# Kernel optimization log

Measured on AMD Instinct MI355X. Metric: run time of the kernel, lower is better.

Reference implementation:

```python
import jax, jax.numpy as jnp
import numpy as np

QLEN, MLEN, BSZ = 1024, 1024, 4
D_MODEL, N_HEAD, D_HEAD, D_INNER = 1024, 16, 64, 4096
KLEN = QLEN + MLEN  # = rlen
LN_EPS = 1e-5


def setup_inputs() -> dict:
    key = jax.random.key(0)
    ks = jax.random.split(key, 16)
    s = 0.02
    nhd = N_HEAD * D_HEAD
    inp = {
        "dec_inp": jax.random.normal(ks[0], (QLEN, BSZ, D_MODEL), jnp.float32),
        "r": jax.random.normal(ks[1], (KLEN, D_MODEL), jnp.float32),
        "r_w_bias": jax.random.normal(ks[2], (N_HEAD, D_HEAD), jnp.float32) * s,
        "r_r_bias": jax.random.normal(ks[3], (N_HEAD, D_HEAD), jnp.float32) * s,
        "mems": jax.random.normal(ks[4], (MLEN, BSZ, D_MODEL), jnp.float32),
        # causal mask with memory: position j visible to query i iff j <= i + MLEN
        "dec_attn_mask": (jnp.arange(KLEN)[None, :] > (jnp.arange(QLEN)[:, None] + MLEN))[:, :, None],
        # parameters
        "qkv_w": jax.random.normal(ks[5], (D_MODEL, 3 * nhd), jnp.float32) * s,
        "r_w": jax.random.normal(ks[6], (D_MODEL, nhd), jnp.float32) * s,
        "o_w": jax.random.normal(ks[7], (nhd, D_MODEL), jnp.float32) * s,
        "ln1_w": jnp.ones((D_MODEL,), jnp.float32),
        "ln1_b": jnp.zeros((D_MODEL,), jnp.float32),
        "ln2_w": jnp.ones((D_MODEL,), jnp.float32),
        "ln2_b": jnp.zeros((D_MODEL,), jnp.float32),
        "ff_w1": jax.random.normal(ks[8], (D_MODEL, D_INNER), jnp.float32) * s,
        "ff_b1": jnp.zeros((D_INNER,), jnp.float32),
        "ff_w2": jax.random.normal(ks[9], (D_INNER, D_MODEL), jnp.float32) * s,
        "ff_b2": jnp.zeros((D_MODEL,), jnp.float32),
    }
    return inp


def _layer_norm(x, w, b):
    mu = jnp.mean(x, axis=-1, keepdims=True)
    var = jnp.mean(jnp.square(x - mu), axis=-1, keepdims=True)
    return (x - mu) * jax.lax.rsqrt(var + LN_EPS) * w + b


def _rel_shift(x):
    # x: [qlen, rlen, bsz, n_head] -- Transformer-XL pad/reshape shift
    q, rl = x.shape[0], x.shape[1]
    zero_pad = jnp.zeros((q, 1) + x.shape[2:], x.dtype)
    x_padded = jnp.concatenate([zero_pad, x], axis=1)
    x_padded = x_padded.reshape((rl + 1, q) + x.shape[2:])
    return x_padded[1:].reshape(x.shape)


def reference(dec_inp, r, r_w_bias, r_r_bias, mems, dec_attn_mask,
              qkv_w, r_w, o_w, ln1_w, ln1_b, ln2_w, ln2_b,
              ff_w1, ff_b1, ff_w2, ff_b2):
    qlen, bsz = dec_inp.shape[0], dec_inp.shape[1]
    nhd = N_HEAD * D_HEAD
    scale = 1.0 / (D_HEAD ** 0.5)

    cat = jnp.concatenate([mems, dec_inp], axis=0)          # [klen, b, d]
    w_heads = cat @ qkv_w                                   # [klen, b, 3*nhd]
    w_head_q, w_head_k, w_head_v = jnp.split(w_heads, 3, axis=-1)
    w_head_q = w_head_q[-qlen:]                             # [qlen, b, nhd]
    klen = w_head_k.shape[0]

    w_head_q = w_head_q.reshape(qlen, bsz, N_HEAD, D_HEAD)
    w_head_k = w_head_k.reshape(klen, bsz, N_HEAD, D_HEAD)
    w_head_v = w_head_v.reshape(klen, bsz, N_HEAD, D_HEAD)
    r_head_k = (r @ r_w).reshape(-1, N_HEAD, D_HEAD)        # [rlen, n, d]

    AC = jnp.einsum('ibnd,jbnd->ijbn', w_head_q + r_w_bias, w_head_k)
    BD = jnp.einsum('ibnd,jnd->ijbn', w_head_q + r_r_bias, r_head_k)
    BD = _rel_shift(BD)

    attn_score = (AC + BD) * scale                          # [q, k, b, n]
    attn_score = jnp.where(dec_attn_mask[:, :, :, None], -jnp.inf, attn_score)
    attn_prob = jax.nn.softmax(attn_score, axis=1)

    attn_vec = jnp.einsum('ijbn,jbnd->ibnd', attn_prob, w_head_v)
    attn_out = attn_vec.reshape(qlen, bsz, nhd) @ o_w       # [q, b, d]

    output = _layer_norm(dec_inp + attn_out, ln1_w, ln1_b)
    ff = jax.nn.relu(output @ ff_w1 + ff_b1) @ ff_w2 + ff_b2
    return _layer_norm(output + ff, ln2_w, ln2_b)
```

## Files before the change

### kernel.cpp

```cpp
#include <hip/hip_runtime.h>
#include <hip/hip_bf16.h>
#include <math.h>

#define QLEN 1024
#define MLEN 1024
#define BSZ 4
#define KLEN 2048
#define NH 16
#define DH 64
#define DM 1024
#define DI 4096
#define NHD 1024
#define LN_EPS 1e-5f

typedef short bf16x8 __attribute__((ext_vector_type(8)));
typedef float f32x4 __attribute__((ext_vector_type(4)));
typedef unsigned int uint4v __attribute__((ext_vector_type(4)));

__device__ __forceinline__ float bf2f(unsigned short u) {
    union { unsigned u32; float f; } x; x.u32 = ((unsigned)u) << 16; return x.f;
}
__device__ __forceinline__ unsigned short f2bf(float f) {
    __hip_bfloat16 h = __float2bfloat16(f);
    return *(unsigned short*)&h;
}

static const size_t OFF_CATB  = 0;
static const size_t OFF_VTG   = 0;
static const size_t OFF_WHB   = 16777216;
static const size_t OFF_RB    = 67108864;
static const size_t OFF_RHKB  = 71303168;
static const size_t OFF_AVB   = 75497472;
static const size_t OFF_TMP   = 83886080;
static const size_t OFF_LN1F  = 100663296;
static const size_t OFF_LN1B  = 117440512;
static const size_t OFF_FFHB  = 125829120;
static const size_t OFF_QKVWT = 159383552;
static const size_t OFF_RWT   = 165675008;
static const size_t OFF_OWT   = 167772160;
static const size_t OFF_FFW1T = 169869312;
static const size_t OFF_FFW2T = 178257920;

__global__ __launch_bounds__(256) void cast_cat(const float* __restrict__ mems,
                                                const float* __restrict__ dec,
                                                unsigned short* __restrict__ out) {
    size_t i8 = ((size_t)blockIdx.x * 256 + threadIdx.x) * 8;
    const size_t half = (size_t)MLEN * BSZ * DM;
    const float* src = (i8 < half) ? (mems + i8) : (dec + (i8 - half));
    float4 v0 = *(const float4*)src;
    float4 v1 = *(const float4*)(src + 4);
    ushort4 o0 = {f2bf(v0.x), f2bf(v0.y), f2bf(v0.z), f2bf(v0.w)};
    ushort4 o1 = {f2bf(v1.x), f2bf(v1.y), f2bf(v1.z), f2bf(v1.w)};
    *(ushort4*)&out[i8] = o0;
    *(ushort4*)&out[i8 + 4] = o1;
}

__global__ __launch_bounds__(256) void cast_f32_bf16(const float* __restrict__ in,
                                                     unsigned short* __restrict__ out) {
    size_t i8 = ((size_t)blockIdx.x * 256 + threadIdx.x) * 8;
    float4 v0 = *(const float4*)(in + i8);
    float4 v1 = *(const float4*)(in + i8 + 4);
    ushort4 o0 = {f2bf(v0.x), f2bf(v0.y), f2bf(v0.z), f2bf(v0.w)};
    ushort4 o1 = {f2bf(v1.x), f2bf(v1.y), f2bf(v1.z), f2bf(v1.w)};
    *(ushort4*)&out[i8] = o0;
    *(ushort4*)&out[i8 + 4] = o1;
}

__global__ __launch_bounds__(256) void transpose_cast_all(
        const float* __restrict__ qkv_w, const float* __restrict__ r_w,
        const float* __restrict__ o_w,  const float* __restrict__ ff_w1,
        const float* __restrict__ ff_w2,
        unsigned short* __restrict__ qkvwT, unsigned short* __restrict__ rwT,
        unsigned short* __restrict__ owT, unsigned short* __restrict__ ffw1T,
        unsigned short* __restrict__ ffw2T) {
    __shared__ float tile[32][33];
    const int bid = blockIdx.x;
    const float* in; unsigned short* out; int K, N, nx, lid;
    if (bid < 3072)      { in = qkv_w; out = qkvwT; K = 1024; N = 3072; nx = 96;  lid = bid; }
    else if (bid < 4096) { in = r_w;   out = rwT;   K = 1024; N = 1024; nx = 32;  lid = bid - 3072; }
    else if (bid < 5120) { in = o_w;   out = owT;   K = 1024; N = 1024; nx = 32;  lid = bid - 4096; }
    else if (bid < 9216) { in = ff_w1; out = ffw1T; K = 1024; N = 4096; nx = 128; lid = bid - 5120; }
    else                 { in = ff_w2; out = ffw2T; K = 4096; N = 1024; nx = 32;  lid = bid - 9216; }
    const int n0 = (lid % nx) * 32;
    const int k0 = (lid / nx) * 32;
    const int t = threadIdx.x;
    const int r = t >> 3;
    const int c0 = (t & 7) << 2;
    float4 v = *(const float4*)&in[(size_t)(k0 + r) * N + n0 + c0];
    tile[r][c0 + 0] = v.x; tile[r][c0 + 1] = v.y;
    tile[r][c0 + 2] = v.z; tile[r][c0 + 3] = v.w;
    __syncthreads();
    ushort4 o = {f2bf(tile[c0 + 0][r]), f2bf(tile[c0 + 1][r]),
                 f2bf(tile[c0 + 2][r]), f2bf(tile[c0 + 3][r])};
    *(ushort4*)&out[(size_t)(n0 + r) * K + k0 + c0] = o;
}

__global__ __launch_bounds__(256) void gemm_bf16(const unsigned short* __restrict__ A,
                                                 const unsigned short* __restrict__ Bt,
                                                 const float* __restrict__ bias,
                                                 void* __restrict__ C,
                                                 int M, int N, int K, int flags) {
    __shared__ __align__(16) unsigned short As[128 * 64];
    __shared__ __align__(16) unsigned short Bs[128 * 64];

    const int tid = threadIdx.x;
    const int w = tid >> 6, l = tid & 63;
    const int wr = w >> 1, wc = w & 1;
    const int row0 = blockIdx.y * 128;
    const int col0 = blockIdx.x * 128;

    f32x4 acc[4][4] = {};

    uint4v ra[4], rb[4];
    {
#pragma unroll
        for (int q = 0; q < 4; ++q) {
            int f = q * 256 + tid, r = f >> 3, c = f & 7;
            ra[q] = *(const uint4v*)&A[(size_t)(row0 + r) * K + c * 8];
            rb[q] = *(const uint4v*)&Bt[(size_t)(col0 + r) * K + c * 8];
        }
    }

    const int nt = K >> 6;
    for (int kt = 0; kt < nt; ++kt) {
        __syncthreads();
#pragma unroll
        for (int q = 0; q < 4; ++q) {
            int f = q * 256 + tid, r = f >> 3, c = f & 7;
            int sw = (c ^ (r & 7)) << 3;
            *(uint4v*)&As[r * 64 + sw] = ra[q];
            *(uint4v*)&Bs[r * 64 + sw] = rb[q];
        }
        __syncthreads();
        if (kt + 1 < nt) {
            const int k0 = (kt + 1) << 6;
#pragma unroll
            for (int q = 0; q < 4; ++q) {
                int f = q * 256 + tid, r = f >> 3, c = f & 7;
                ra[q] = *(const uint4v*)&A[(size_t)(row0 + r) * K + k0 + c * 8];
                rb[q] = *(const uint4v*)&Bt[(size_t)(col0 + r) * K + k0 + c * 8];
            }
        }
#pragma unroll
        for (int ks = 0; ks < 2; ++ks) {
            bf16x8 a[4], bfr[4];
#pragma unroll
            for (int m = 0; m < 4; ++m) {
                int arow = wr * 64 + m * 16 + (l & 15);
                int chunk = (ks * 4 + (l >> 4)) ^ (arow & 7);
                a[m] = *(const bf16x8*)&As[arow * 64 + chunk * 8];
            }
#pragma unroll
            for (int n = 0; n < 4; ++n) {
                int brow = wc * 64 + n * 16 + (l & 15);
                int chunk = (ks * 4 + (l >> 4)) ^ (brow & 7);
                bfr[n] = *(const bf16x8*)&Bs[brow * 64 + chunk * 8];
            }
#pragma unroll
            for (int m = 0; m < 4; ++m)
#pragma unroll
                for (int n = 0; n < 4; ++n)
                    acc[m][n] = __builtin_amdgcn_mfma_f32_16x16x32_bf16(a[m], bfr[n], acc[m][n], 0, 0, 0);
        }
    }

#pragma unroll
    for (int n = 0; n < 4; ++n) {
        const int ccol = col0 + wc * 64 + n * 16 + (l & 15);
        const float bv = (flags & 1) ? bias[ccol] : 0.0f;
#pragma unroll
        for (int m = 0; m < 4; ++m) {
            const int crow0 = row0 + wr * 64 + m * 16 + ((l >> 4) << 2);
#pragma unroll
            for (int reg = 0; reg < 4; ++reg) {
                float v = acc[m][n][reg] + bv;
                if (flags & 2) v = fmaxf(v, 0.0f);
                if (flags & 4)
                    ((unsigned short*)C)[(size_t)(crow0 + reg) * N + ccol] = f2bf(v);
                else
                    ((float*)C)[(size_t)(crow0 + reg) * N + ccol] = v;
            }
        }
    }
}

__global__ __launch_bounds__(256) void vtrans(const unsigned short* __restrict__ whb,
                                              unsigned short* __restrict__ vtg) {
    __shared__ unsigned short tile[64][72];
    const int bn = blockIdx.y;
    const int b = bn >> 4, n = bn & 15, nb = n * 64;
    const int jt0 = blockIdx.x * 64;
    const int tid = threadIdx.x;
#pragma unroll
    for (int g = 0; g < 2; ++g) {
        int f = g * 256 + tid;
        int key = f >> 3, c = f & 7;
        uint4v v = *(const uint4v*)&whb[((size_t)(jt0 + key) * 4 + b) * 3072 + 2048 + nb + c * 8];
        *(uint4v*)&tile[key][c * 8] = v;
    }
    __syncthreads();
#pragma unroll
    for (int g = 0; g < 2; ++g) {
        int f = g * 256 + tid;
        int d = f >> 3, ck = f & 7;
        unsigned short tmp[8];
#pragma unroll
        for (int e = 0; e < 8; ++e) tmp[e] = tile[ck * 8 + e][d];
        *(uint4v*)&vtg[(size_t)bn * 131072 + (size_t)d * 2048 + jt0 + ck * 8] = *(uint4v*)tmp;
    }
}

__global__ __launch_bounds__(512) void flash_attn_mfma(const unsigned short* __restrict__ whb,
                                                       const unsigned short* __restrict__ rhkb,
                                                       const unsigned short* __restrict__ vtg,
                                                       const float* __restrict__ r_w_bias,
                                                       const float* __restrict__ r_r_bias,
                                                       unsigned short* __restrict__ avb) {
    const int bid = blockIdx.x;
    const int bn = bid >> 3;
    const int z = bid & 7;
    const int bx = (z & 1) ? (z >> 1) : 7 - (z >> 1);
    const int b = bn >> 4, n = bn & 15, nb = n * 64;
    const int i0 = bx << 7;
    const int tid = threadIdx.x;
    const int wq = tid >> 6;
    const int lane = tid & 63;
    const int rg = lane >> 4;
    const int lc = lane & 15;
    const int m7 = lc & 7;

    __shared__ __align__(16) unsigned short Ks[4096];
    __shared__ __align__(16) unsigned short Rs[16384];
    __shared__ __align__(16) unsigned short Vt[4096];
    __shared__ __align__(16) unsigned short SCR[8][1408];

    bf16x8 qac0, qac1, qbd0, qbd1;
    {
        const int qrow = MLEN + i0 + wq * 16 + lc;
        const unsigned short* qp = whb + ((size_t)qrow * 4 + b) * 3072 + nb + rg * 8;
        bf16x8 q0 = *(const bf16x8*)(qp);
        bf16x8 q1 = *(const bf16x8*)(qp + 32);
        const float* wbp = r_w_bias + nb + rg * 8;
        const float* rbp = r_r_bias + nb + rg * 8;
#pragma unroll
        for (int e = 0; e < 8; ++e) {
            const float v0 = bf2f((unsigned short)q0[e]);
            const float v1 = bf2f((unsigned short)q1[e]);
            qac0[e] = (short)f2bf((v0 + wbp[e]) * 0.125f);
            qbd0[e] = (short)f2bf((v0 + rbp[e]) * 0.125f);
            qac1[e] = (short)f2bf((v1 + wbp[32 + e]) * 0.125f);
            qbd1[e] = (short)f2bf((v1 + rbp[32 + e]) * 0.125f);
        }
    }

    f32x4 Oacc[4] = {};
    float mrun = -INFINITY, lrun = 0.f;

    const int ntiles = 2 * bx + 18;
    const int wbase_off = 112 - 16 * wq;

    const int srow = tid >> 3;
    const int sc = tid & 7;
    unsigned short* scr = &SCR[wq][0];

    uint4v pk, pv, pr3[3];
    {
        pk = *(const uint4v*)&whb[((size_t)srow * 4 + b) * 3072 + 1024 + nb + sc * 8];
        pv = *(const uint4v*)&vtg[(size_t)bn * 131072 + (size_t)srow * 2048 + sc * 8];
        const int relbase0 = 896 - i0;
#pragma unroll
        for (int p = 0; p < 3; ++p) {
            const int a = relbase0 + p * 64 + srow;
            pr3[p] = *(const uint4v*)&rhkb[(size_t)a * 1024 + nb + sc * 8];
        }
    }

    for (int kt = 0; kt < ntiles; ++kt) {
        const int jt0 = kt << 6;
        const int relbase = jt0 - i0 + 896;
        __syncthreads();

        *(uint4v*)&Ks[srow * 64 + ((sc ^ (srow & 7)) << 3)] = pk;
        *(uint4v*)&Vt[srow * 64 + ((sc ^ (srow & 7)) << 3)] = pv;
        if (kt == 0) {
#pragma unroll
            for (int p = 0; p < 3; ++p) {
                const int a = relbase + p * 64 + srow;
                const int dst = ((a >> 6) & 3) * 4096 + (a & 63) * 64 + ((sc ^ (a & 7)) << 3);
                *(uint4v*)&Rs[dst] = pr3[p];
            }
        } else {
            const int a = relbase + 128 + srow;
            const int dst = ((a >> 6) & 3) * 4096 + (a & 63) * 64 + ((sc ^ (a & 7)) << 3);
            *(uint4v*)&Rs[dst] = pr3[0];
        }
        if (kt + 1 < ntiles) {
            const int jn = jt0 + 64;
            pk = *(const uint4v*)&whb[((size_t)(jn + srow) * 4 + b) * 3072 + 1024 + nb + sc * 8];
            pv = *(const uint4v*)&vtg[(size_t)bn * 131072 + (size_t)srow * 2048 + jn + sc * 8];
            int a = relbase + 192 + srow;
            if (a > 2047) a = 2047;
            pr3[0] = *(const uint4v*)&rhkb[(size_t)a * 1024 + nb + sc * 8];
        }
        __syncthreads();

        f32x4 S[4];
        __builtin_amdgcn_s_setprio(1);
#pragma unroll
        for (int nf = 0; nf < 4; ++nf) {
            const int row = nf * 16 + lc;
            const bf16x8 kf0 = *(const bf16x8*)&Ks[row * 64 + ((rg ^ m7) << 3)];
            const bf16x8 kf1 = *(const bf16x8*)&Ks[row * 64 + (((4 + rg) ^ m7) << 3)];
            f32x4 zz = {0.f, 0.f, 0.f, 0.f};
            zz = __builtin_amdgcn_mfma_f32_16x16x32_bf16(kf0, qac0, zz, 0, 0, 0);
            S[nf] = __builtin_amdgcn_mfma_f32_16x16x32_bf16(kf1, qac1, zz, 0, 0, 0);
        }
        __builtin_amdgcn_s_setprio(0);

        const int wbase = relbase + wbase_off;
#pragma unroll
        for (int g = 0; g < 5; ++g) {
            const int a = wbase + g * 16 + lc;
            const int rbase = ((a >> 6) & 3) * 4096 + (a & 63) * 64;
            const bf16x8 rf0 = *(const bf16x8*)&Rs[rbase + ((rg ^ m7) << 3)];
            const bf16x8 rf1 = *(const bf16x8*)&Rs[rbase + (((4 + rg) ^ m7) << 3)];
            f32x4 bd = {0.f, 0.f, 0.f, 0.f};
            bd = __builtin_amdgcn_mfma_f32_16x16x32_bf16(rf0, qbd0, bd, 0, 0, 0);
            bd = __builtin_amdgcn_mfma_f32_16x16x32_bf16(rf1, qbd1, bd, 0, 0, 0);
            ushort4 p4 = {f2bf(bd[0]), f2bf(bd[1]), f2bf(bd[2]), f2bf(bd[3])};
            *(ushort4*)&scr[lc * 88 + g * 16 + rg * 4] = p4;
        }

        const bool needmask = (wbase + 78 > 2047);
        float tmax = -INFINITY;
#pragma unroll
        for (int nf = 0; nf < 4; ++nf) {
#pragma unroll
            for (int r = 0; r < 4; ++r) {
                const int wb_ = 15 + nf * 16 + rg * 4 + r - lc;
                float s = S[nf][r] + bf2f(scr[lc * 88 + wb_]);
                if (needmask) s = (wbase + wb_ <= 2047) ? s : -INFINITY;
                S[nf][r] = s;
                tmax = fmaxf(tmax, s);
            }
        }

        tmax = fmaxf(tmax, __shfl_xor(tmax, 16));
        tmax = fmaxf(tmax, __shfl_xor(tmax, 32));
        const float mn = fmaxf(mrun, tmax);
        const float ef = __expf(mrun - mn);
        mrun = mn;
        float rsum = 0.f;
#pragma unroll
        for (int nf = 0; nf < 4; ++nf) {
#pragma unroll
            for (int r = 0; r < 4; ++r) {
                const float p = __expf(S[nf][r] - mn);
                S[nf][r] = p;
                rsum += p;
            }
        }
        rsum += __shfl_xor(rsum, 16);
        rsum += __shfl_xor(rsum, 32);
        lrun = lrun * ef + rsum;
        if (__any(ef < 1.0f)) {
#pragma unroll
            for (int nf = 0; nf < 4; ++nf)
#pragma unroll
                for (int r = 0; r < 4; ++r) Oacc[nf][r] *= ef;
        }

#pragma unroll
        for (int nf = 0; nf < 4; ++nf) {
            ushort4 pw = {f2bf(S[nf][0]), f2bf(S[nf][1]), f2bf(S[nf][2]), f2bf(S[nf][3])};
            const int chunk = nf * 2 + (rg >> 1);
            *(ushort4*)&scr[lc * 88 + ((chunk ^ m7) << 3) + ((rg & 1) << 2)] = pw;
        }

        {
            const bf16x8 pf0 = *(const bf16x8*)&scr[lc * 88 + ((rg ^ m7) << 3)];
            const bf16x8 pf1 = *(const bf16x8*)&scr[lc * 88 + (((4 + rg) ^ m7) << 3)];
            __builtin_amdgcn_s_setprio(1);
#pragma unroll
            for (int nf = 0; nf < 4; ++nf) {
                const int row = nf * 16 + lc;
                const bf16x8 vf0 = *(const bf16x8*)&Vt[row * 64 + ((rg ^ m7) << 3)];
                const bf16x8 vf1 = *(const bf16x8*)&Vt[row * 64 + (((4 + rg) ^ m7) << 3)];
                Oacc[nf] = __builtin_amdgcn_mfma_f32_16x16x32_bf16(vf0, pf0, Oacc[nf], 0, 0, 0);
                Oacc[nf] = __builtin_amdgcn_mfma_f32_16x16x32_bf16(vf1, pf1, Oacc[nf], 0, 0, 0);
            }
            __builtin_amdgcn_s_setprio(0);
        }
    }

    const float inv = 1.0f / lrun;
    const int qg = i0 + wq * 16 + lc;
#pragma unroll
    for (int nf = 0; nf < 4; ++nf) {
        ushort4 o = {f2bf(Oacc[nf][0] * inv), f2bf(Oacc[nf][1] * inv),
                     f2bf(Oacc[nf][2] * inv), f2bf(Oacc[nf][3] * inv)};
        *(ushort4*)&avb[((size_t)qg * 4 + b) * 1024 + nb + nf * 16 + rg * 4] = o;
    }
}

__global__ __launch_bounds__(256) void add_ln_kernel(const float* __restrict__ a,
                                                     const float* __restrict__ b,
                                                     const float* __restrict__ w,
                                                     const float* __restrict__ bias,
                                                     float* __restrict__ out,
                                                     unsigned short* __restrict__ out_bf) {
    const int row = blockIdx.x;
    const int t = threadIdx.x;
    const int c0 = t << 2;
    __shared__ float red[256];

    const float4 av = *(const float4*)&a[(size_t)row * DM + c0];
    const float4 bv = *(const float4*)&b[(size_t)row * DM + c0];
    float x0 = av.x + bv.x, x1 = av.y + bv.y, x2 = av.z + bv.z, x3 = av.w + bv.w;

    red[t] = x0 + x1 + x2 + x3;
    __syncthreads();
    for (int off = 128; off > 0; off >>= 1) {
        if (t < off) red[t] += red[t + off];
        __syncthreads();
    }
    const float mu = red[0] * (1.0f / DM);
    __syncthreads();

    const float d0 = x0 - mu, d1 = x1 - mu, d2 = x2 - mu, d3 = x3 - mu;
    red[t] = d0 * d0 + d1 * d1 + d2 * d2 + d3 * d3;
    __syncthreads();
    for (int off = 128; off > 0; off >>= 1) {
        if (t < off) red[t] += red[t + off];
        __syncthreads();
    }
    const float rstd = rsqrtf(red[0] * (1.0f / DM) + LN_EPS);

    const float4 wv = *(const float4*)&w[c0];
    const float4 bsv = *(const float4*)&bias[c0];
    float4 o = {d0 * rstd * wv.x + bsv.x, d1 * rstd * wv.y + bsv.y,
                d2 * rstd * wv.z + bsv.z, d3 * rstd * wv.w + bsv.w};
    *(float4*)&out[(size_t)row * DM + c0] = o;
    if (out_bf) {
        ushort4 ob = {f2bf(o.x), f2bf(o.y), f2bf(o.z), f2bf(o.w)};
        *(ushort4*)&out_bf[(size_t)row * DM + c0] = ob;
    }
}

extern "C" void kernel_launch(void* const* d_in, const int* in_sizes, int n_in,
                              void* d_out, int out_size, void* d_ws, size_t ws_size,
                              hipStream_t stream) {
    const float* dec_inp  = (const float*)d_in[0];
    const float* r        = (const float*)d_in[1];
    const float* r_w_bias = (const float*)d_in[2];
    const float* r_r_bias = (const float*)d_in[3];
    const float* mems     = (const float*)d_in[4];
    const float* qkv_w    = (const float*)d_in[6];
    const float* r_w      = (const float*)d_in[7];
    const float* o_w      = (const float*)d_in[8];
    const float* ln1_w    = (const float*)d_in[9];
    const float* ln1_b    = (const float*)d_in[10];
    const float* ln2_w    = (const float*)d_in[11];
    const float* ln2_b    = (const float*)d_in[12];
    const float* ff_w1    = (const float*)d_in[13];
    const float* ff_b1    = (const float*)d_in[14];
    const float* ff_w2    = (const float*)d_in[15];
    const float* ff_b2    = (const float*)d_in[16];
    float* out = (float*)d_out;
    char* ws = (char*)d_ws;

    unsigned short* catb  = (unsigned short*)(ws + OFF_CATB);
    unsigned short* vtg   = (unsigned short*)(ws + OFF_VTG);
    unsigned short* whb   = (unsigned short*)(ws + OFF_WHB);
    unsigned short* rb    = (unsigned short*)(ws + OFF_RB);
    unsigned short* rhkb  = (unsigned short*)(ws + OFF_RHKB);
    unsigned short* avb   = (unsigned short*)(ws + OFF_AVB);
    float*          tmp   = (float*)(ws + OFF_TMP);
    float*          ln1f  = (float*)(ws + OFF_LN1F);
    unsigned short* ln1b  = (unsigned short*)(ws + OFF_LN1B);
    unsigned short* ffhb  = (unsigned short*)(ws + OFF_FFHB);
    unsigned short* qkvwT = (unsigned short*)(ws + OFF_QKVWT);
    unsigned short* rwT   = (unsigned short*)(ws + OFF_RWT);
    unsigned short* owT   = (unsigned short*)(ws + OFF_OWT);
    unsigned short* ffw1T = (unsigned short*)(ws + OFF_FFW1T);
    unsigned short* ffw2T = (unsigned short*)(ws + OFF_FFW2T);

    cast_cat<<<dim3(4096), 256, 0, stream>>>(mems, dec_inp, catb);
    cast_f32_bf16<<<dim3(1024), 256, 0, stream>>>(r, rb);
    transpose_cast_all<<<dim3(13312), 256, 0, stream>>>(
        qkv_w, r_w, o_w, ff_w1, ff_w2, qkvwT, rwT, owT, ffw1T, ffw2T);

    gemm_bf16<<<dim3(24, 64), 256, 0, stream>>>(catb, qkvwT, nullptr, whb,
                                                KLEN * BSZ, 3 * NHD, DM, 4);
    gemm_bf16<<<dim3(8, 16), 256, 0, stream>>>(rb, rwT, nullptr, rhkb,
                                               KLEN, NHD, DM, 4);

    vtrans<<<dim3(32, 64), 256, 0, stream>>>(whb, vtg);

    flash_attn_mfma<<<dim3(512), 512, 0, stream>>>(
        whb, rhkb, vtg, r_w_bias, r_r_bias, avb);

    gemm_bf16<<<dim3(8, 32), 256, 0, stream>>>(avb, owT, nullptr, tmp,
                                               QLEN * BSZ, DM, NHD, 0);
    add_ln_kernel<<<dim3(QLEN * BSZ), 256, 0, stream>>>(
        dec_inp, tmp, ln1_w, ln1_b, ln1f, ln1b);
    gemm_bf16<<<dim3(32, 32), 256, 0, stream>>>(ln1b, ffw1T, ff_b1, ffhb,
                                                QLEN * BSZ, DI, DM, 1 | 2 | 4);
    gemm_bf16<<<dim3(8, 32), 256, 0, stream>>>(ffhb, ffw2T, ff_b2, tmp,
                                               QLEN * BSZ, DM, DI, 1);
    add_ln_kernel<<<dim3(QLEN * BSZ), 256, 0, stream>>>(
        ln1f, tmp, ln2_w, ln2_b, out, nullptr);
}
```

Baseline: 402.8 us.

## Load K, V and R MFMA fragments directly from global memory, dropping LDS staging

The attention kernel no longer stages K, V^T and relative-position R tiles through shared memory with register prefetch and two block barriers per tile. Each wave now reads its MFMA operand fragments straight from global memory, clamping R indices at the end of the sequence. This removes the barriers and LDS traffic but makes the 8 waves each re-read the same K/V/R data from cache/HBM, with strided, less coalesced accesses and no software prefetch.

Measured after the change: 623.2 us. +54.7%, slower.

```diff
diff --git a/kernel.cpp b/kernel.cpp
--- a/kernel.cpp
+++ b/kernel.cpp
@@ -229,9 +229,6 @@
     const int lc = lane & 15;
     const int m7 = lc & 7;
 
-    __shared__ __align__(16) unsigned short Ks[4096];
-    __shared__ __align__(16) unsigned short Rs[16384];
-    __shared__ __align__(16) unsigned short Vt[4096];
     __shared__ __align__(16) unsigned short SCR[8][1408];
 
     bf16x8 qac0, qac1, qbd0, qbd1;
@@ -258,72 +255,37 @@
 
     const int ntiles = 2 * bx + 18;
     const int wbase_off = 112 - 16 * wq;
-
-    const int srow = tid >> 3;
-    const int sc = tid & 7;
     unsigned short* scr = &SCR[wq][0];
 
-    uint4v pk, pv, pr3[3];
-    {
-        pk = *(const uint4v*)&whb[((size_t)srow * 4 + b) * 3072 + 1024 + nb + sc * 8];
-        pv = *(const uint4v*)&vtg[(size_t)bn * 131072 + (size_t)srow * 2048 + sc * 8];
-        const int relbase0 = 896 - i0;
-#pragma unroll
-        for (int p = 0; p < 3; ++p) {
-            const int a = relbase0 + p * 64 + srow;
-            pr3[p] = *(const uint4v*)&rhkb[(size_t)a * 1024 + nb + sc * 8];
-        }
-    }
+    const unsigned short* kfrag = whb + (size_t)b * 3072 + 1024 + nb + rg * 8 + (size_t)lc * 12288;
+    const unsigned short* vfrag = vtg + (size_t)bn * 131072 + (size_t)lc * 2048 + rg * 8;
+    const unsigned short* rfrag = rhkb + nb + rg * 8;
 
     for (int kt = 0; kt < ntiles; ++kt) {
         const int jt0 = kt << 6;
         const int relbase = jt0 - i0 + 896;
-        __syncthreads();
-
-        *(uint4v*)&Ks[srow * 64 + ((sc ^ (srow & 7)) << 3)] = pk;
-        *(uint4v*)&Vt[srow * 64 + ((sc ^ (srow & 7)) << 3)] = pv;
-        if (kt == 0) {
-#pragma unroll
-            for (int p = 0; p < 3; ++p) {
-                const int a = relbase + p * 64 + srow;
-                const int dst = ((a >> 6) & 3) * 4096 + (a & 63) * 64 + ((sc ^ (a & 7)) << 3);
-                *(uint4v*)&Rs[dst] = pr3[p];
-            }
-        } else {
-            const int a = relbase + 128 + srow;
-            const int dst = ((a >> 6) & 3) * 4096 + (a & 63) * 64 + ((sc ^ (a & 7)) << 3);
-            *(uint4v*)&Rs[dst] = pr3[0];
-        }
-        if (kt + 1 < ntiles) {
-            const int jn = jt0 + 64;
-            pk = *(const uint4v*)&whb[((size_t)(jn + srow) * 4 + b) * 3072 + 1024 + nb + sc * 8];
-            pv = *(const uint4v*)&vtg[(size_t)bn * 131072 + (size_t)srow * 2048 + jn + sc * 8];
-            int a = relbase + 192 + srow;
-            if (a > 2047) a = 2047;
-            pr3[0] = *(const uint4v*)&rhkb[(size_t)a * 1024 + nb + sc * 8];
-        }
-        __syncthreads();
+        const int wbase = relbase + wbase_off;
 
         f32x4 S[4];
         __builtin_amdgcn_s_setprio(1);
 #pragma unroll
         for (int nf = 0; nf < 4; ++nf) {
-            const int row = nf * 16 + lc;
-            const bf16x8 kf0 = *(const bf16x8*)&Ks[row * 64 + ((rg ^ m7) << 3)];
-            const bf16x8 kf1 = *(const bf16x8*)&Ks[row * 64 + (((4 + rg) ^ m7) << 3)];
+            const unsigned short* kp = kfrag + (size_t)(jt0 + nf * 16) * 12288;
+            const bf16x8 kf0 = *(const bf16x8*)(kp);
+            const bf16x8 kf1 = *(const bf16x8*)(kp + 32);
             f32x4 zz = {0.f, 0.f, 0.f, 0.f};
             zz = __builtin_amdgcn_mfma_f32_16x16x32_bf16(kf0, qac0, zz, 0, 0, 0);
             S[nf] = __builtin_amdgcn_mfma_f32_16x16x32_bf16(kf1, qac1, zz, 0, 0, 0);
         }
         __builtin_amdgcn_s_setprio(0);
 
-        const int wbase = relbase + wbase_off;
 #pragma unroll
         for (int g = 0; g < 5; ++g) {
-            const int a = wbase + g * 16 + lc;
-            const int rbase = ((a >> 6) & 3) * 4096 + (a & 63) * 64;
-            const bf16x8 rf0 = *(const bf16x8*)&Rs[rbase + ((rg ^ m7) << 3)];
-            const bf16x8 rf1 = *(const bf16x8*)&Rs[rbase + (((4 + rg) ^ m7) << 3)];
+            int a = wbase + g * 16 + lc;
+            if (a > 2047) a = 2047;
+            const unsigned short* rp = rfrag + (size_t)a * 1024;
+            const bf16x8 rf0 = *(const bf16x8*)(rp);
+            const bf16x8 rf1 = *(const bf16x8*)(rp + 32);
             f32x4 bd = {0.f, 0.f, 0.f, 0.f};
             bd = __builtin_amdgcn_mfma_f32_16x16x32_bf16(rf0, qbd0, bd, 0, 0, 0);
             bd = __builtin_amdgcn_mfma_f32_16x16x32_bf16(rf1, qbd1, bd, 0, 0, 0);
@@ -383,9 +345,9 @@
             __builtin_amdgcn_s_setprio(1);
 #pragma unroll
             for (int nf = 0; nf < 4; ++nf) {
-                const int row = nf * 16 + lc;
-                const bf16x8 vf0 = *(const bf16x8*)&Vt[row * 64 + ((rg ^ m7) << 3)];
-                const bf16x8 vf1 = *(const bf16x8*)&Vt[row * 64 + (((4 + rg) ^ m7) << 3)];
+                const unsigned short* vp = vfrag + (size_t)(nf * 16) * 2048 + jt0;
+                const bf16x8 vf0 = *(const bf16x8*)(vp);
+                const bf16x8 vf1 = *(const bf16x8*)(vp + 32);
                 Oacc[nf] = __builtin_amdgcn_mfma_f32_16x16x32_bf16(vf0, pf0, Oacc[nf], 0, 0, 0);
                 Oacc[nf] = __builtin_amdgcn_mfma_f32_16x16x32_bf16(vf1, pf1, Oacc[nf], 0, 0, 0);
             }
```

## Split attention key range into two halves per block with merge kernel

Applied to the files above, without the earlier changes.

Each attention block now handles two jobs. Each job covers half the key tiles of a query block, and the jobs pair a short query block with a long one so work is balanced. Partial unnormalized outputs and running max/sum are written in fp32 and combined by a new merge kernel. The pairing is meant to fix load imbalance from the causal triangle, at the cost of extra fp32 partial traffic and one more kernel launch. The o-proj and FF2 GEMMs also now write bf16 intermediates instead of fp32, which lowers bandwidth but loses some precision.

Measured after the change: 396.2 us. No clear change (-1.6%).

```diff
diff --git a/kernel.cpp b/kernel.cpp
--- a/kernel.cpp
+++ b/kernel.cpp
@@ -31,7 +31,8 @@
 static const size_t OFF_RB    = 67108864;
 static const size_t OFF_RHKB  = 71303168;
 static const size_t OFF_AVB   = 75497472;
-static const size_t OFF_TMP   = 83886080;
+static const size_t OFF_TMPB  = 83886080;
+static const size_t OFF_ML    = 92274688;
 static const size_t OFF_LN1F  = 100663296;
 static const size_t OFF_LN1B  = 117440512;
 static const size_t OFF_FFHB  = 125829120;
@@ -215,13 +216,12 @@
                                                        const unsigned short* __restrict__ vtg,
                                                        const float* __restrict__ r_w_bias,
                                                        const float* __restrict__ r_r_bias,
-                                                       unsigned short* __restrict__ avb) {
+                                                       float* __restrict__ opart,
+                                                       float* __restrict__ ml) {
     const int bid = blockIdx.x;
     const int bn = bid >> 3;
-    const int z = bid & 7;
-    const int bx = (z & 1) ? (z >> 1) : 7 - (z >> 1);
+    const int kk0 = bid & 7;
     const int b = bn >> 4, n = bn & 15, nb = n * 64;
-    const int i0 = bx << 7;
     const int tid = threadIdx.x;
     const int wq = tid >> 6;
     const int lane = tid & 63;
@@ -234,177 +234,215 @@
     __shared__ __align__(16) unsigned short Vt[4096];
     __shared__ __align__(16) unsigned short SCR[8][1408];
 
-    bf16x8 qac0, qac1, qbd0, qbd1;
-    {
-        const int qrow = MLEN + i0 + wq * 16 + lc;
-        const unsigned short* qp = whb + ((size_t)qrow * 4 + b) * 3072 + nb + rg * 8;
-        bf16x8 q0 = *(const bf16x8*)(qp);
-        bf16x8 q1 = *(const bf16x8*)(qp + 32);
-        const float* wbp = r_w_bias + nb + rg * 8;
-        const float* rbp = r_r_bias + nb + rg * 8;
-#pragma unroll
-        for (int e = 0; e < 8; ++e) {
-            const float v0 = bf2f((unsigned short)q0[e]);
-            const float v1 = bf2f((unsigned short)q1[e]);
-            qac0[e] = (short)f2bf((v0 + wbp[e]) * 0.125f);
-            qbd0[e] = (short)f2bf((v0 + rbp[e]) * 0.125f);
-            qac1[e] = (short)f2bf((v1 + wbp[32 + e]) * 0.125f);
-            qbd1[e] = (short)f2bf((v1 + rbp[32 + e]) * 0.125f);
-        }
-    }
-
-    f32x4 Oacc[4] = {};
-    float mrun = -INFINITY, lrun = 0.f;
-
-    const int ntiles = 2 * bx + 18;
     const int wbase_off = 112 - 16 * wq;
-
     const int srow = tid >> 3;
     const int sc = tid & 7;
     unsigned short* scr = &SCR[wq][0];
 
-    uint4v pk, pv, pr3[3];
-    {
-        pk = *(const uint4v*)&whb[((size_t)srow * 4 + b) * 3072 + 1024 + nb + sc * 8];
-        pv = *(const uint4v*)&vtg[(size_t)bn * 131072 + (size_t)srow * 2048 + sc * 8];
-        const int relbase0 = 896 - i0;
-#pragma unroll
-        for (int p = 0; p < 3; ++p) {
-            const int a = relbase0 + p * 64 + srow;
-            pr3[p] = *(const uint4v*)&rhkb[(size_t)a * 1024 + nb + sc * 8];
-        }
-    }
-
-    for (int kt = 0; kt < ntiles; ++kt) {
-        const int jt0 = kt << 6;
-        const int relbase = jt0 - i0 + 896;
-        __syncthreads();
-
-        *(uint4v*)&Ks[srow * 64 + ((sc ^ (srow & 7)) << 3)] = pk;
-        *(uint4v*)&Vt[srow * 64 + ((sc ^ (srow & 7)) << 3)] = pv;
-        if (kt == 0) {
+    for (int job = 0; job < 2; ++job) {
+        const int h = job;
+        const int bx = job ? (7 - kk0) : kk0;
+        const int i0 = bx << 7;
+        const int halfn = bx + 9;
+        const int kt0 = h * halfn;
+        const int ktend = kt0 + halfn;
+
+        bf16x8 qac0, qac1, qbd0, qbd1;
+        {
+            const int qrow = MLEN + i0 + wq * 16 + lc;
+            const unsigned short* qp = whb + ((size_t)qrow * 4 + b) * 3072 + nb + rg * 8;
+            bf16x8 q0 = *(const bf16x8*)(qp);
+            bf16x8 q1 = *(const bf16x8*)(qp + 32);
+            const float* wbp = r_w_bias + nb + rg * 8;
+            const float* rbp = r_r_bias + nb + rg * 8;
+#pragma unroll
+            for (int e = 0; e < 8; ++e) {
+                const float v0 = bf2f((unsigned short)q0[e]);
+                const float v1 = bf2f((unsigned short)q1[e]);
+                qac0[e] = (short)f2bf((v0 + wbp[e]) * 0.125f);
+                qbd0[e] = (short)f2bf((v0 + rbp[e]) * 0.125f);
+                qac1[e] = (short)f2bf((v1 + wbp[32 + e]) * 0.125f);
+                qbd1[e] = (short)f2bf((v1 + rbp[32 + e]) * 0.125f);
+            }
+        }
+
+        f32x4 Oacc[4] = {};
+        float mrun = -INFINITY, lrun = 0.f;
+
+        uint4v pk, pv, pr3[3];
+        {
+            const int j0 = kt0 << 6;
+            pk = *(const uint4v*)&whb[((size_t)(j0 + srow) * 4 + b) * 3072 + 1024 + nb + sc * 8];
+            pv = *(const uint4v*)&vtg[(size_t)bn * 131072 + (size_t)srow * 2048 + j0 + sc * 8];
+            const int relst = j0 - i0 + 896;
 #pragma unroll
             for (int p = 0; p < 3; ++p) {
-                const int a = relbase + p * 64 + srow;
+                int a = relst + p * 64 + srow;
+                if (a > 2047) a = 2047;
+                pr3[p] = *(const uint4v*)&rhkb[(size_t)a * 1024 + nb + sc * 8];
+            }
+        }
+
+        for (int kt = kt0; kt < ktend; ++kt) {
+            const int jt0 = kt << 6;
+            const int relbase = jt0 - i0 + 896;
+            __syncthreads();
+
+            *(uint4v*)&Ks[srow * 64 + ((sc ^ (srow & 7)) << 3)] = pk;
+            *(uint4v*)&Vt[srow * 64 + ((sc ^ (srow & 7)) << 3)] = pv;
+            if (kt == kt0) {
+#pragma unroll
+                for (int p = 0; p < 3; ++p) {
+                    int a = relbase + p * 64 + srow;
+                    if (a > 2047) a = 2047;
+                    const int dst = ((a >> 6) & 3) * 4096 + (a & 63) * 64 + ((sc ^ (a & 7)) << 3);
+                    *(uint4v*)&Rs[dst] = pr3[p];
+                }
+            } else {
+                int a = relbase + 128 + srow;
+                if (a > 2047) a = 2047;
                 const int dst = ((a >> 6) & 3) * 4096 + (a & 63) * 64 + ((sc ^ (a & 7)) << 3);
-                *(uint4v*)&Rs[dst] = pr3[p];
-            }
-        } else {
-            const int a = relbase + 128 + srow;
-            const int dst = ((a >> 6) & 3) * 4096 + (a & 63) * 64 + ((sc ^ (a & 7)) << 3);
-            *(uint4v*)&Rs[dst] = pr3[0];
-        }
-        if (kt + 1 < ntiles) {
-            const int jn = jt0 + 64;
-            pk = *(const uint4v*)&whb[((size_t)(jn + srow) * 4 + b) * 3072 + 1024 + nb + sc * 8];
-            pv = *(const uint4v*)&vtg[(size_t)bn * 131072 + (size_t)srow * 2048 + jn + sc * 8];
-            int a = relbase + 192 + srow;
-            if (a > 2047) a = 2047;
-            pr3[0] = *(const uint4v*)&rhkb[(size_t)a * 1024 + nb + sc * 8];
-        }
-        __syncthreads();
-
-        f32x4 S[4];
-        __builtin_amdgcn_s_setprio(1);
-#pragma unroll
-        for (int nf = 0; nf < 4; ++nf) {
-            const int row = nf * 16 + lc;
-            const bf16x8 kf0 = *(const bf16x8*)&Ks[row * 64 + ((rg ^ m7) << 3)];
-            const bf16x8 kf1 = *(const bf16x8*)&Ks[row * 64 + (((4 + rg) ^ m7) << 3)];
-            f32x4 zz = {0.f, 0.f, 0.f, 0.f};
-            zz = __builtin_amdgcn_mfma_f32_16x16x32_bf16(kf0, qac0, zz, 0, 0, 0);
-            S[nf] = __builtin_amdgcn_mfma_f32_16x16x32_bf16(kf1, qac1, zz, 0, 0, 0);
-        }
-        __builtin_amdgcn_s_setprio(0);
-
-        const int wbase = relbase + wbase_off;
-#pragma unroll
-        for (int g = 0; g < 5; ++g) {
-            const int a = wbase + g * 16 + lc;
-            const int rbase = ((a >> 6) & 3) * 4096 + (a & 63) * 64;
-            const bf16x8 rf0 = *(const bf16x8*)&Rs[rbase + ((rg ^ m7) << 3)];
-            const bf16x8 rf1 = *(const bf16x8*)&Rs[rbase + (((4 + rg) ^ m7) << 3)];
-            f32x4 bd = {0.f, 0.f, 0.f, 0.f};
-            bd = __builtin_amdgcn_mfma_f32_16x16x32_bf16(rf0, qbd0, bd, 0, 0, 0);
-            bd = __builtin_amdgcn_mfma_f32_16x16x32_bf16(rf1, qbd1, bd, 0, 0, 0);
-            ushort4 p4 = {f2bf(bd[0]), f2bf(bd[1]), f2bf(bd[2]), f2bf(bd[3])};
-            *(ushort4*)&scr[lc * 88 + g * 16 + rg * 4] = p4;
-        }
-
-        const bool needmask = (wbase + 78 > 2047);
-        float tmax = -INFINITY;
-#pragma unroll
-        for (int nf = 0; nf < 4; ++nf) {
-#pragma unroll
-            for (int r = 0; r < 4; ++r) {
-                const int wb_ = 15 + nf * 16 + rg * 4 + r - lc;
-                float s = S[nf][r] + bf2f(scr[lc * 88 + wb_]);
-                if (needmask) s = (wbase + wb_ <= 2047) ? s : -INFINITY;
-                S[nf][r] = s;
-                tmax = fmaxf(tmax, s);
-            }
-        }
-
-        tmax = fmaxf(tmax, __shfl_xor(tmax, 16));
-        tmax = fmaxf(tmax, __shfl_xor(tmax, 32));
-        const float mn = fmaxf(mrun, tmax);
-        const float ef = __expf(mrun - mn);
-        mrun = mn;
-        float rsum = 0.f;
-#pragma unroll
-        for (int nf = 0; nf < 4; ++nf) {
-#pragma unroll
-            for (int r = 0; r < 4; ++r) {
-                const float p = __expf(S[nf][r] - mn);
-                S[nf][r] = p;
-                rsum += p;
-            }
-        }
-        rsum += __shfl_xor(rsum, 16);
-        rsum += __shfl_xor(rsum, 32);
-        lrun = lrun * ef + rsum;
-        if (__any(ef < 1.0f)) {
-#pragma unroll
-            for (int nf = 0; nf < 4; ++nf)
-#pragma unroll
-                for (int r = 0; r < 4; ++r) Oacc[nf][r] *= ef;
-        }
-
-#pragma unroll
-        for (int nf = 0; nf < 4; ++nf) {
-            ushort4 pw = {f2bf(S[nf][0]), f2bf(S[nf][1]), f2bf(S[nf][2]), f2bf(S[nf][3])};
-            const int chunk = nf * 2 + (rg >> 1);
-            *(ushort4*)&scr[lc * 88 + ((chunk ^ m7) << 3) + ((rg & 1) << 2)] = pw;
-        }
-
-        {
-            const bf16x8 pf0 = *(const bf16x8*)&scr[lc * 88 + ((rg ^ m7) << 3)];
-            const bf16x8 pf1 = *(const bf16x8*)&scr[lc * 88 + (((4 + rg) ^ m7) << 3)];
+                *(uint4v*)&Rs[dst] = pr3[0];
+            }
+            if (kt + 1 < ktend) {
+                const int jn = jt0 + 64;
+                pk = *(const uint4v*)&whb[((size_t)(jn + srow) * 4 + b) * 3072 + 1024 + nb + sc * 8];
+                pv = *(const uint4v*)&vtg[(size_t)bn * 131072 + (size_t)srow * 2048 + jn + sc * 8];
+                int a = relbase + 192 + srow;
+                if (a > 2047) a = 2047;
+                pr3[0] = *(const uint4v*)&rhkb[(size_t)a * 1024 + nb + sc * 8];
+            }
+            __syncthreads();
+
+            f32x4 S[4];
             __builtin_amdgcn_s_setprio(1);
 #pragma unroll
             for (int nf = 0; nf < 4; ++nf) {
                 const int row = nf * 16 + lc;
-                const bf16x8 vf0 = *(const bf16x8*)&Vt[row * 64 + ((rg ^ m7) << 3)];
-                const bf16x8 vf1 = *(const bf16x8*)&Vt[row * 64 + (((4 + rg) ^ m7) << 3)];
-                Oacc[nf] = __builtin_amdgcn_mfma_f32_16x16x32_bf16(vf0, pf0, Oacc[nf], 0, 0, 0);
-                Oacc[nf] = __builtin_amdgcn_mfma_f32_16x16x32_bf16(vf1, pf1, Oacc[nf], 0, 0, 0);
+                const bf16x8 kf0 = *(const bf16x8*)&Ks[row * 64 + ((rg ^ m7) << 3)];
+                const bf16x8 kf1 = *(const bf16x8*)&Ks[row * 64 + (((4 + rg) ^ m7) << 3)];
+                f32x4 zz = {0.f, 0.f, 0.f, 0.f};
+                zz = __builtin_amdgcn_mfma_f32_16x16x32_bf16(kf0, qac0, zz, 0, 0, 0);
+                S[nf] = __builtin_amdgcn_mfma_f32_16x16x32_bf16(kf1, qac1, zz, 0, 0, 0);
             }
             __builtin_amdgcn_s_setprio(0);
-        }
-    }
-
-    const float inv = 1.0f / lrun;
-    const int qg = i0 + wq * 16 + lc;
-#pragma unroll
-    for (int nf = 0; nf < 4; ++nf) {
-        ushort4 o = {f2bf(Oacc[nf][0] * inv), f2bf(Oacc[nf][1] * inv),
-                     f2bf(Oacc[nf][2] * inv), f2bf(Oacc[nf][3] * inv)};
-        *(ushort4*)&avb[((size_t)qg * 4 + b) * 1024 + nb + nf * 16 + rg * 4] = o;
-    }
+
+            const int wbase = relbase + wbase_off;
+#pragma unroll
+            for (int g = 0; g < 5; ++g) {
+                const int a = wbase + g * 16 + lc;
+                const int rbase = ((a >> 6) & 3) * 4096 + (a & 63) * 64;
+                const bf16x8 rf0 = *(const bf16x8*)&Rs[rbase + ((rg ^ m7) << 3)];
+                const bf16x8 rf1 = *(const bf16x8*)&Rs[rbase + (((4 + rg) ^ m7) << 3)];
+                f32x4 bd = {0.f, 0.f, 0.f, 0.f};
+                bd = __builtin_amdgcn_mfma_f32_16x16x32_bf16(rf0, qbd0, bd, 0, 0, 0);
+                bd = __builtin_amdgcn_mfma_f32_16x16x32_bf16(rf1, qbd1, bd, 0, 0, 0);
+                ushort4 p4 = {f2bf(bd[0]), f2bf(bd[1]), f2bf(bd[2]), f2bf(bd[3])};
+                *(ushort4*)&scr[lc * 88 + g * 16 + rg * 4] = p4;
+            }
+
+            const bool needmask = (wbase + 78 > 2047);
+            float tmax = -INFINITY;
+#pragma unroll
+            for (int nf = 0; nf < 4; ++nf) {
+#pragma unroll
+                for (int r = 0; r < 4; ++r) {
+                    const int wb_ = 15 + nf * 16 + rg * 4 + r - lc;
+                    float s = S[nf][r] + bf2f(scr[lc * 88 + wb_]);
+                    if (needmask) s = (wbase + wb_ <= 2047) ? s : -INFINITY;
+                    S[nf][r] = s;
+                    tmax = fmaxf(tmax, s);
+                }
+            }
+
+            tmax = fmaxf(tmax, __shfl_xor(tmax, 16));
+            tmax = fmaxf(tmax, __shfl_xor(tmax, 32));
+            const float mn = fmaxf(mrun, tmax);
+            const float ef = __expf(mrun - mn);
+            mrun = mn;
+            float rsum = 0.f;
+#pragma unroll
+            for (int nf = 0; nf < 4; ++nf) {
+#pragma unroll
+                for (int r = 0; r < 4; ++r) {
+                    const float p = __expf(S[nf][r] - mn);
+                    S[nf][r] = p;
+                    rsum += p;
+                }
+            }
+            rsum += __shfl_xor(rsum, 16);
+            rsum += __shfl_xor(rsum, 32);
+            lrun = lrun * ef + rsum;
+            if (__any(ef < 1.0f)) {
+#pragma unroll
+                for (int nf = 0; nf < 4; ++nf)
+#pragma unroll
+                    for (int r = 0; r < 4; ++r) Oacc[nf][r] *= ef;
+            }
+
+#pragma unroll
+            for (int nf = 0; nf < 4; ++nf) {
+                ushort4 pw = {f2bf(S[nf][0]), f2bf(S[nf][1]), f2bf(S[nf][2]), f2bf(S[nf][3])};
+                const int chunk = nf * 2 + (rg >> 1);
+                *(ushort4*)&scr[lc * 88 + ((chunk ^ m7) << 3) + ((rg & 1) << 2)] = pw;
+            }
+
+            {
+                const bf16x8 pf0 = *(const bf16x8*)&scr[lc * 88 + ((rg ^ m7) << 3)];
+                const bf16x8 pf1 = *(const bf16x8*)&scr[lc * 88 + (((4 + rg) ^ m7) << 3)];
+                __builtin_amdgcn_s_setprio(1);
+#pragma unroll
+                for (int nf = 0; nf < 4; ++nf) {
+                    const int row = nf * 16 + lc;
+                    const bf16x8 vf0 = *(const bf16x8*)&Vt[row * 64 + ((rg ^ m7) << 3)];
+                    const bf16x8 vf1 = *(const bf16x8*)&Vt[row * 64 + (((4 + rg) ^ m7) << 3)];
+                    Oacc[nf] = __builtin_amdgcn_mfma_f32_16x16x32_bf16(vf0, pf0, Oacc[nf], 0, 0, 0);
+                    Oacc[nf] = __builtin_amdgcn_mfma_f32_16x16x32_bf16(vf1, pf1, Oacc[nf], 0, 0, 0);
+                }
+                __builtin_amdgcn_s_setprio(0);
+            }
+        }
+
+        const int qg = i0 + wq * 16 + lc;
+        const int rowf = qg * 4 + b;
+        float* op = opart + (size_t)h * 4194304 + (size_t)rowf * 1024 + nb;
+#pragma unroll
+        for (int nf = 0; nf < 4; ++nf) {
+            float4 o = {Oacc[nf][0], Oacc[nf][1], Oacc[nf][2], Oacc[nf][3]};
+            *(float4*)&op[nf * 16 + rg * 4] = o;
+        }
+        if (rg == 0) {
+            float* mp = ml + (size_t)h * 131072 + ((size_t)rowf * 16 + n) * 2;
+            mp[0] = mrun;
+            mp[1] = lrun;
+        }
+    }
+}
+
+__global__ __launch_bounds__(256) void merge_attn(const float* __restrict__ opart,
+                                                  const float* __restrict__ ml,
+                                                  unsigned short* __restrict__ avb) {
+    const size_t g = (size_t)blockIdx.x * 256 + threadIdx.x;
+    const size_t c4 = g << 2;
+    const int row = (int)(c4 >> 10);
+    const int col = (int)(c4 & 1023);
+    const int n = col >> 6;
+    const size_t mlb = ((size_t)row * 16 + n) * 2;
+    const float m1 = ml[mlb], l1 = ml[mlb + 1];
+    const float m2 = ml[131072 + mlb], l2 = ml[131072 + mlb + 1];
+    const float m = fmaxf(m1, m2);
+    const float e1 = __expf(m1 - m), e2 = __expf(m2 - m);
+    const float inv = 1.0f / (e1 * l1 + e2 * l2);
+    const float s1 = e1 * inv, s2 = e2 * inv;
+    const float4 o1 = *(const float4*)&opart[c4];
+    const float4 o2 = *(const float4*)&opart[4194304 + c4];
+    ushort4 o = {f2bf(o1.x * s1 + o2.x * s2), f2bf(o1.y * s1 + o2.y * s2),
+                 f2bf(o1.z * s1 + o2.z * s2), f2bf(o1.w * s1 + o2.w * s2)};
+    *(ushort4*)&avb[c4] = o;
 }
 
 __global__ __launch_bounds__(256) void add_ln_kernel(const float* __restrict__ a,
-                                                     const float* __restrict__ b,
+                                                     const unsigned short* __restrict__ b,
                                                      const float* __restrict__ w,
                                                      const float* __restrict__ bias,
                                                      float* __restrict__ out,
@@ -415,8 +453,9 @@
     __shared__ float red[256];
 
     const float4 av = *(const float4*)&a[(size_t)row * DM + c0];
-    const float4 bv = *(const float4*)&b[(size_t)row * DM + c0];
-    float x0 = av.x + bv.x, x1 = av.y + bv.y, x2 = av.z + bv.z, x3 = av.w + bv.w;
+    const ushort4 bu = *(const ushort4*)&b[(size_t)row * DM + c0];
+    float x0 = av.x + bf2f(bu.x), x1 = av.y + bf2f(bu.y);
+    float x2 = av.z + bf2f(bu.z), x3 = av.w + bf2f(bu.w);
 
     red[t] = x0 + x1 + x2 + x3;
     __syncthreads();
@@ -475,10 +514,12 @@
     unsigned short* rb    = (unsigned short*)(ws + OFF_RB);
     unsigned short* rhkb  = (unsigned short*)(ws + OFF_RHKB);
     unsigned short* avb   = (unsigned short*)(ws + OFF_AVB);
-    float*          tmp   = (float*)(ws + OFF_TMP);
+    unsigned short* tmpb  = (unsigned short*)(ws + OFF_TMPB);
+    float*          mlbuf = (float*)(ws + OFF_ML);
     float*          ln1f  = (float*)(ws + OFF_LN1F);
     unsigned short* ln1b  = (unsigned short*)(ws + OFF_LN1B);
     unsigned short* ffhb  = (unsigned short*)(ws + OFF_FFHB);
+    float*          opart = (float*)(ws + OFF_FFHB);
     unsigned short* qkvwT = (unsigned short*)(ws + OFF_QKVWT);
     unsigned short* rwT   = (unsigned short*)(ws + OFF_RWT);
     unsigned short* owT   = (unsigned short*)(ws + OFF_OWT);
@@ -498,16 +539,17 @@
     vtrans<<<dim3(32, 64), 256, 0, stream>>>(whb, vtg);
 
     flash_attn_mfma<<<dim3(512), 512, 0, stream>>>(
-        whb, rhkb, vtg, r_w_bias, r_r_bias, avb);
-
-    gemm_bf16<<<dim3(8, 32), 256, 0, stream>>>(avb, owT, nullptr, tmp,
-                                               QLEN * BSZ, DM, NHD, 0);
+        whb, rhkb, vtg, r_w_bias, r_r_bias, opart, mlbuf);
+    merge_attn<<<dim3(4096), 256, 0, stream>>>(opart, mlbuf, avb);
+
+    gemm_bf16<<<dim3(8, 32), 256, 0, stream>>>(avb, owT, nullptr, tmpb,
+                                               QLEN * BSZ, DM, NHD, 4);
     add_ln_kernel<<<dim3(QLEN * BSZ), 256, 0, stream>>>(
-        dec_inp, tmp, ln1_w, ln1_b, ln1f, ln1b);
+        dec_inp, tmpb, ln1_w, ln1_b, ln1f, ln1b);
     gemm_bf16<<<dim3(32, 32), 256, 0, stream>>>(ln1b, ffw1T, ff_b1, ffhb,
                                                 QLEN * BSZ, DI, DM, 1 | 2 | 4);
-    gemm_bf16<<<dim3(8, 32), 256, 0, stream>>>(ffhb, ffw2T, ff_b2, tmp,
-                                               QLEN * BSZ, DM, DI, 1);
+    gemm_bf16<<<dim3(8, 32), 256, 0, stream>>>(ffhb, ffw2T, ff_b2, tmpb,
+                                               QLEN * BSZ, DM, DI, 1 | 4);
     add_ln_kernel<<<dim3(QLEN * BSZ), 256, 0, stream>>>(
-        ln1f, tmp, ln2_w, ln2_b, out, nullptr);
-}
+        ln1f, tmpb, ln2_w, ln2_b, out, nullptr);
+}
```
